# Kernel tuning notes

Measured on AMD Instinct MI355X. Metric: run time of the kernel, lower is better.

The kernel has to match this reference:

```python
import jax, jax.numpy as jnp
import numpy as np

B, T, D, H, V = 256, 32, 500, 1024, 8000
NF = 512  # conv output channels per window size


def setup_inputs() -> dict:
    key = jax.random.key(0)
    ks = jax.random.split(key, 20)
    s = 0.02
    inp = {
        "text": jax.random.normal(ks[0], (B, T, D), jnp.float32),
        "text_bow": jax.random.uniform(ks[1], (B, V), jnp.float32),
        "text_lengths": jax.random.randint(ks[2], (B,), 1, T + 1).astype(jnp.int32),
        # GRU forward direction (PyTorch layout: [3H, D], [3H, H], gates r,z,n)
        "Wih_f": jax.random.normal(ks[3], (3 * H, D), jnp.float32) * s,
        "Whh_f": jax.random.normal(ks[4], (3 * H, H), jnp.float32) * s,
        "bih_f": jax.random.normal(ks[5], (3 * H,), jnp.float32) * s,
        "bhh_f": jax.random.normal(ks[6], (3 * H,), jnp.float32) * s,
        # GRU backward direction
        "Wih_b": jax.random.normal(ks[7], (3 * H, D), jnp.float32) * s,
        "Whh_b": jax.random.normal(ks[8], (3 * H, H), jnp.float32) * s,
        "bih_b": jax.random.normal(ks[9], (3 * H,), jnp.float32) * s,
        "bhh_b": jax.random.normal(ks[10], (3 * H,), jnp.float32) * s,
        # reduce linear: 2H -> H
        "W_red": jax.random.normal(ks[11], (H, 2 * H), jnp.float32) * s,
        "b_red": jax.random.normal(ks[12], (H,), jnp.float32) * s,
        # conv kernels, reshaped from Conv2d [512,1,ws,2H] to 1D conv [512, 2H, ws]
        "conv_w2": jax.random.normal(ks[13], (NF, 2 * H, 2), jnp.float32) * s,
        "conv_b2": jax.random.normal(ks[14], (NF,), jnp.float32) * s,
        "conv_w3": jax.random.normal(ks[15], (NF, 2 * H, 3), jnp.float32) * s,
        "conv_b3": jax.random.normal(ks[16], (NF,), jnp.float32) * s,
        "conv_w4": jax.random.normal(ks[17], (NF, 2 * H, 4), jnp.float32) * s,
        "conv_b4": jax.random.normal(ks[18], (NF,), jnp.float32) * s,
    }
    return inp


def _run_gru_dir(x, lengths, Wih, Whh, bih, bhh, reverse):
    """One GRU direction over padded [B,T,D] with packed-sequence semantics:
    outputs are zero at t >= length (as pad_packed_sequence produces)."""
    b, t, _ = x.shape
    h_dim = Whh.shape[1]
    xg = jnp.einsum('btd,gd->btg', x, Wih) + bih  # [B,T,3H] input projections
    valid = jnp.arange(t)[None, :] < lengths[:, None]  # [B,T]

    def step(h, inp):
        xg_t, v = inp  # [B,3H], [B]
        hg = h @ Whh.T + bhh
        xr, xz, xn = jnp.split(xg_t, 3, axis=-1)
        hr, hz, hn = jnp.split(hg, 3, axis=-1)
        r = jax.nn.sigmoid(xr + hr)
        z = jax.nn.sigmoid(xz + hz)
        n = jnp.tanh(xn + r * hn)
        h_new = (1.0 - z) * n + z * h
        h_new = jnp.where(v[:, None], h_new, h)
        out = jnp.where(v[:, None], h_new, 0.0)
        return h_new, out

    h0 = jnp.zeros((b, h_dim), x.dtype)
    xs = (jnp.swapaxes(xg, 0, 1), valid.T)  # time-major
    _, outs = jax.lax.scan(step, h0, xs, reverse=reverse)
    return jnp.swapaxes(outs, 0, 1)  # [B,T,H]


def _conv_branch(x_c, w, b, ws):
    # x_c: [B, 2H, T]; w: [512, 2H, ws]; 'same-padding-both-sides' (ws-1) like Conv2d padding=(ws-1,0)
    y = jax.lax.conv_general_dilated(
        x_c, w, window_strides=(1,), padding=[(ws - 1, ws - 1)],
        dimension_numbers=('NCH', 'OIH', 'NCH')) + b[None, :, None]
    y = jax.nn.leaky_relu(y, 0.01)
    return jnp.max(y, axis=-1)  # global max-pool over time -> [B,512]


def reference(text, text_bow, text_lengths, Wih_f, Whh_f, bih_f, bhh_f,
              Wih_b, Whh_b, bih_b, bhh_b, W_red, b_red,
              conv_w2, conv_b2, conv_w3, conv_b3, conv_w4, conv_b4):
    out_f = _run_gru_dir(text, text_lengths, Wih_f, Whh_f, bih_f, bhh_f, reverse=False)
    out_b = _run_gru_dir(text, text_lengths, Wih_b, Whh_b, bih_b, bhh_b, reverse=True)
    gru_init_out = jnp.concatenate([out_f, out_b], axis=-1)  # [B,T,2H]

    # masked mean pooling over valid timesteps (the per-sample Python loop)
    mask = (jnp.arange(gru_init_out.shape[1])[None, :] < text_lengths[:, None]).astype(gru_init_out.dtype)
    gru_mean = jnp.sum(gru_init_out * mask[:, :, None], axis=1) / text_lengths[:, None].astype(gru_init_out.dtype)
    gru_out = gru_mean @ W_red.T + b_red  # [B,H] (dropout is identity at eval)

    x_c = jnp.swapaxes(gru_init_out, 1, 2)  # [B,2H,T]
    con_out = jnp.concatenate([
        _conv_branch(x_c, conv_w2, conv_b2, 2),
        _conv_branch(x_c, conv_w3, conv_b3, 3),
        _conv_branch(x_c, conv_w4, conv_b4, 4),
    ], axis=1)  # [B,1536]

    return jnp.concatenate([gru_out, con_out, text_bow], axis=1)  # [B, H+1536+V]
```

## Files before the change

kernel.cpp:

```cpp
#include <hip/hip_runtime.h>
#include <hip/hip_bf16.h>
#include <math.h>

#define B_ 256
#define T_ 32
#define D_ 500
#define H_ 1024
#define V_ 8000
#define NF_ 512
#define G3H (3*H_)
#define G6H (6*H_)
#define H2 (2*H_)
#define OUTC (H_ + 3*NF_ + V_)
#define KPAD 512
#define NTAP 9
#define NCAT (NTAP*NF_)
#define MS 512
#define WFRAG_G (64*32*512)
#define WHH_N (3*64*32*64)

typedef float f32x4 __attribute__((ext_vector_type(4)));
typedef short bf16x8 __attribute__((ext_vector_type(8)));

static __device__ __forceinline__ short f2b(float f) {
    unsigned u = __float_as_uint(f);
    unsigned r = (u + 0x7fffu + ((u >> 16) & 1u)) >> 16;
    return (short)r;
}
static __device__ __forceinline__ float b2f(short s) {
    return __uint_as_float(((unsigned)(unsigned short)s) << 16);
}

template<int MODE>
__global__ __launch_bounds__(256) void gemm_bt2(
    const short* __restrict__ A, int lda,
    const short* __restrict__ Bt, int ldb,
    const float* __restrict__ bias,
    void* __restrict__ Cv, int ldc, int K)
{
    __shared__ short As[3][128 * 32];
    __shared__ short Bs[3][128 * 32];
    const int tid = threadIdx.x;
    const int w = tid >> 6, lane = tid & 63;

    const int nbx = gridDim.x;
    const int nwg = nbx * gridDim.y;
    const int C = nwg >> 3;
    const int R = gridDim.y >> 3;
    const int orig = blockIdx.y * nbx + blockIdx.x;
    const int x = orig & 7;
    const int local = orig >> 3;
    const int seg = local / (R * 4);
    const int rem = local % (R * 4);
    const int mm = rem >> 2, nn = rem & 3;
    const int m0 = (x * R + mm) * 128;
    const int n0 = (seg * 4 + nn) * 128;

    const int wm = (w >> 1) * 64, wn = (w & 1) * 64;

    const int sa = lane & 1, sb = (lane >> 1) & 1, sc = (lane >> 2) & 1;
    const int sd = (lane >> 3) & 1, se = (lane >> 4) & 1, sg = (lane >> 5) & 1;
    const int srow = w * 16 + (sc ^ sg) + 2 * sd + 4 * se + 8 * sg;
    const int scol = 8 * ((sa ^ sd) + 2 * (sb ^ se));
    const long aoff0 = (long)(m0 + srow) * lda + scol;
    const long aoff1 = (long)(m0 + srow + 64) * lda + scol;
    const long boff0 = (long)(n0 + srow) * ldb + scol;
    const long boff1 = (long)(n0 + srow + 64) * ldb + scol;

#define STG(t_) do { \
    const int bu_ = (t_) % 3; \
    const long ka_ = (long)(t_) * 32; \
    __builtin_amdgcn_global_load_lds((const __attribute__((address_space(1))) void*)(A + aoff0 + ka_), \
        (__attribute__((address_space(3))) void*)(&As[bu_][w * 512]), 16, 0, 0); \
    __builtin_amdgcn_global_load_lds((const __attribute__((address_space(1))) void*)(A + aoff1 + ka_), \
        (__attribute__((address_space(3))) void*)(&As[bu_][2048 + w * 512]), 16, 0, 0); \
    __builtin_amdgcn_global_load_lds((const __attribute__((address_space(1))) void*)(Bt + boff0 + ka_), \
        (__attribute__((address_space(3))) void*)(&Bs[bu_][w * 512]), 16, 0, 0); \
    __builtin_amdgcn_global_load_lds((const __attribute__((address_space(1))) void*)(Bt + boff1 + ka_), \
        (__attribute__((address_space(3))) void*)(&Bs[bu_][2048 + w * 512]), 16, 0, 0); \
} while (0)

    f32x4 acc[4][4];
#pragma unroll
    for (int i = 0; i < 4; ++i)
#pragma unroll
        for (int j = 0; j < 4; ++j) acc[i][j] = (f32x4){0.f, 0.f, 0.f, 0.f};

    const int fr = lane & 15;
    const int fkb = (lane >> 4) * 16;
    const int fxor = ((fr >> 1) & 7) << 4;
    const int T = K >> 5;

    STG(0); STG(1);
    asm volatile("s_waitcnt vmcnt(4)" ::: "memory");
    __builtin_amdgcn_s_barrier();

    for (int t = 0; t < T; ++t) {
        const int bu = t % 3;
        const char* Ab = (const char*)&As[bu][0];
        const char* Bb = (const char*)&Bs[bu][0];

        bf16x8 af[4], bfv[4];
#pragma unroll
        for (int i = 0; i < 4; ++i)
            af[i] = *(const bf16x8*)(Ab + ((((wm + i * 16 + fr) << 6) + fkb) ^ fxor));
#pragma unroll
        for (int j = 0; j < 4; ++j)
            bfv[j] = *(const bf16x8*)(Bb + ((((wn + j * 16 + fr) << 6) + fkb) ^ fxor));

        if (t + 2 < T) STG(t + 2);

#pragma unroll
        for (int i = 0; i < 4; ++i)
#pragma unroll
            for (int j = 0; j < 4; ++j)
                acc[i][j] = __builtin_amdgcn_mfma_f32_16x16x32_bf16(af[i], bfv[j], acc[i][j], 0, 0, 0);

        if (t + 2 < T)      asm volatile("s_waitcnt vmcnt(4)" ::: "memory");
        else if (t + 1 < T) asm volatile("s_waitcnt vmcnt(0)" ::: "memory");
        __builtin_amdgcn_s_barrier();
    }
#undef STG

    const int er = (lane >> 4) * 4, ec = lane & 15;
#pragma unroll
    for (int i = 0; i < 4; ++i) {
#pragma unroll
        for (int j = 0; j < 4; ++j) {
#pragma unroll
            for (int q = 0; q < 4; ++q) {
                const int m = m0 + wm + i * 16 + er + q;
                const int n = n0 + wn + j * 16 + ec;
                const float v = acc[i][j][q];
                if (MODE == 2)
                    ((short*)Cv)[(long)m * ldc + n] = f2b(v + bias[n]);
                else
                    ((_Float16*)Cv)[(long)m * ldc + n] = (_Float16)v;
            }
        }
    }
}

__global__ __launch_bounds__(256) void gemm_bt(
    const short* __restrict__ A, int lda,
    const short* __restrict__ Bt, int ldb,
    const float* __restrict__ bias,
    void* __restrict__ Cv, int ldc,
    int K, int mode)
{
    __shared__ short As[128 * 32];
    __shared__ short Bs[128 * 32];
    const int tid  = threadIdx.x;
    const int w    = tid >> 6, lane = tid & 63;

    const int nbx = gridDim.x;
    const int nwg = nbx * gridDim.y;
    int flat = blockIdx.y * nbx + blockIdx.x;
    flat = (flat & 7) * (nwg >> 3) + (flat >> 3);
    const int m0 = (flat / nbx) * 128, n0 = (flat % nbx) * 128;

    const int wm   = (w >> 1) * 64, wn = (w & 1) * 64;

    f32x4 acc[4][4];
#pragma unroll
    for (int i = 0; i < 4; ++i)
#pragma unroll
        for (int j = 0; j < 4; ++j) acc[i][j] = (f32x4){0.f, 0.f, 0.f, 0.f};

    const int srow = w * 16 + (lane >> 2);
    const int scol = (lane & 3) * 8;
    const long aoff0 = (long)(m0 + srow) * lda + scol;
    const long aoff1 = (long)(m0 + srow + 64) * lda + scol;
    const long boff0 = (long)(n0 + srow) * ldb + scol;
    const long boff1 = (long)(n0 + srow + 64) * ldb + scol;
    short* lA0 = As + w * 512;        short* lA1 = As + 2048 + w * 512;
    short* lB0 = Bs + w * 512;        short* lB1 = Bs + 2048 + w * 512;

    const int fr = lane & 15, fk = (lane >> 4) * 8;

    for (int kt = 0; kt < K; kt += 32) {
        __builtin_amdgcn_global_load_lds((const __attribute__((address_space(1))) void*)(A + aoff0 + kt),
                                         (__attribute__((address_space(3))) void*)lA0, 16, 0, 0);
        __builtin_amdgcn_global_load_lds((const __attribute__((address_space(1))) void*)(A + aoff1 + kt),
                                         (__attribute__((address_space(3))) void*)lA1, 16, 0, 0);
        __builtin_amdgcn_global_load_lds((const __attribute__((address_space(1))) void*)(Bt + boff0 + kt),
                                         (__attribute__((address_space(3))) void*)lB0, 16, 0, 0);
        __builtin_amdgcn_global_load_lds((const __attribute__((address_space(1))) void*)(Bt + boff1 + kt),
                                         (__attribute__((address_space(3))) void*)lB1, 16, 0, 0);
        __syncthreads();
        bf16x8 af[4], bfv[4];
#pragma unroll
        for (int i = 0; i < 4; ++i) af[i]  = *(const bf16x8*)(As + (wm + i * 16 + fr) * 32 + fk);
#pragma unroll
        for (int j = 0; j < 4; ++j) bfv[j] = *(const bf16x8*)(Bs + (wn + j * 16 + fr) * 32 + fk);
#pragma unroll
        for (int i = 0; i < 4; ++i)
#pragma unroll
            for (int j = 0; j < 4; ++j)
                acc[i][j] = __builtin_amdgcn_mfma_f32_16x16x32_bf16(af[i], bfv[j], acc[i][j], 0, 0, 0);
        __syncthreads();
    }

    const int er = (lane >> 4) * 4;
    const int ec = lane & 15;
#pragma unroll
    for (int i = 0; i < 4; ++i) {
#pragma unroll
        for (int j = 0; j < 4; ++j) {
#pragma unroll
            for (int q = 0; q < 4; ++q) {
                const int m = m0 + wm + i * 16 + er + q;
                const int n = n0 + wn + j * 16 + ec;
                float v = acc[i][j][q];
                if (mode == 0) {
                    ((float*)Cv)[(long)m * ldc + n] = v + bias[n];
                } else if (mode == 2) {
                    ((short*)Cv)[(long)m * ldc + n] = f2b(v + bias[n]);
                } else {
                    ((_Float16*)Cv)[(long)m * ldc + n] = (_Float16)v;
                }
            }
        }
    }
}

__global__ void repack_whh2(const float* __restrict__ srcf,
                            const float* __restrict__ srcb,
                            short* __restrict__ dst)
{
    const int idx = blockIdx.x * 256 + threadIdx.x;
    const int h = idx >= WHH_N;
    const int local = idx - h * WHH_N;
    const float* src = h ? srcb : srcf;
    const int l = local & 63;
    const int kt = (local >> 6) & 31;
    const int j16 = (local >> 11) & 63;
    const int g = local >> 17;
    const long srow = ((long)(g << 10) + (j16 << 4) + (l & 15)) * H_ + kt * 32 + ((l >> 4) << 3);
    short o[8];
#pragma unroll
    for (int e = 0; e < 8; ++e) o[e] = f2b(src[srow + e]);
    *(bf16x8*)&dst[(long)idx * 8] = *(bf16x8*)o;
}

__global__ __launch_bounds__(512) void gru_step_frag(
    const short* __restrict__ hbf_prev, short* __restrict__ hbf_next,
    const float* __restrict__ h32_prev, float* __restrict__ h32_next,
    const short* __restrict__ wfragf, const short* __restrict__ wfragb,
    const float* __restrict__ bhhf, const float* __restrict__ bhhb,
    const short* __restrict__ xgcat,
    short* __restrict__ gout, const int* __restrict__ lengths, int s)
{
    __shared__ f32x4 lacc[4][6][64];
    const int tid = threadIdx.x;
    const int w8 = tid >> 6;
    const int w = w8 & 3;
    const int khalf = w8 >> 2;
    const int lane = tid & 63;
    const int bid = blockIdx.x;
    const int jt = bid & 31;
    const int mtd = bid >> 5;
    const int dir = mtd >> 2, mt = mtd & 3;
    const int m0 = dir * 256 + mt * 64;
    const int j0 = jt * 32;
    const int wm = (w >> 1) * 32, wj = (w & 1) * 16;
    const int tt = dir ? (T_ - 1 - s) : s;

    const short* wfrag = dir ? wfragb : wfragf;
    const float* bhh = dir ? bhhb : bhhf;

    const int fr15 = lane & 15, fk8 = (lane >> 4) * 8;
    const long arow0 = (long)(m0 + wm + fr15) * H_ + fk8 + khalf * 512;
    const long arow1 = arow0 + (long)16 * H_;
    const int j16 = (j0 + wj) >> 4;
    const short* bbase = wfrag + ((long)j16 * 32 + khalf * 16) * 512 + lane * 8;

    f32x4 acc[3][2];
#pragma unroll
    for (int g = 0; g < 3; ++g)
#pragma unroll
        for (int i = 0; i < 2; ++i) acc[g][i] = (f32x4){0.f, 0.f, 0.f, 0.f};

#pragma unroll 4
    for (int kt = 0; kt < 16; ++kt) {
        const bf16x8 af0 = *(const bf16x8*)(hbf_prev + arow0 + kt * 32);
        const bf16x8 af1 = *(const bf16x8*)(hbf_prev + arow1 + kt * 32);
        const bf16x8 b0 = *(const bf16x8*)(bbase + (long)kt * 512);
        const bf16x8 b1 = *(const bf16x8*)(bbase + (long)kt * 512 + WFRAG_G);
        const bf16x8 b2 = *(const bf16x8*)(bbase + (long)kt * 512 + 2 * WFRAG_G);
        acc[0][0] = __builtin_amdgcn_mfma_f32_16x16x32_bf16(af0, b0, acc[0][0], 0, 0, 0);
        acc[0][1] = __builtin_amdgcn_mfma_f32_16x16x32_bf16(af1, b0, acc[0][1], 0, 0, 0);
        acc[1][0] = __builtin_amdgcn_mfma_f32_16x16x32_bf16(af0, b1, acc[1][0], 0, 0, 0);
        acc[1][1] = __builtin_amdgcn_mfma_f32_16x16x32_bf16(af1, b1, acc[1][1], 0, 0, 0);
        acc[2][0] = __builtin_amdgcn_mfma_f32_16x16x32_bf16(af0, b2, acc[2][0], 0, 0, 0);
        acc[2][1] = __builtin_amdgcn_mfma_f32_16x16x32_bf16(af1, b2, acc[2][1], 0, 0, 0);
    }

    if (khalf == 1) {
#pragma unroll
        for (int g = 0; g < 3; ++g)
#pragma unroll
            for (int i = 0; i < 2; ++i)
                lacc[w][g * 2 + i][lane] = acc[g][i];
    }
    __syncthreads();
    if (khalf == 1) return;

#pragma unroll
    for (int g = 0; g < 3; ++g)
#pragma unroll
        for (int i = 0; i < 2; ++i)
            acc[g][i] += lacc[w][g * 2 + i][lane];

    const int er = (lane >> 4) * 4, ec = lane & 15;
    const int jj = j0 + wj + ec;
    const float bhr = bhh[jj], bhz = bhh[H_ + jj], bhn = bhh[2 * H_ + jj];

#pragma unroll
    for (int i = 0; i < 2; ++i) {
#pragma unroll
        for (int q = 0; q < 4; ++q) {
            const int m = m0 + wm + i * 16 + er + q;
            const int b = m & 255;
            const short* xrow = xgcat + ((long)b * T_ + tt) * G6H + (long)dir * G3H;
            const float xr = b2f(xrow[jj]);
            const float xz = b2f(xrow[H_ + jj]);
            const float xn = b2f(xrow[2 * H_ + jj]);
            const float rr = 1.f / (1.f + expf(-(xr + acc[0][i][q] + bhr)));
            const float zz = 1.f / (1.f + expf(-(xz + acc[1][i][q] + bhz)));
            const float nn = tanhf(xn + rr * (acc[2][i][q] + bhn));
            const long hidx = (long)m * H_ + jj;
            const float hp = h32_prev[hidx];
            const float hnew = (1.f - zz) * nn + zz * hp;
            const bool valid = tt < lengths[b];
            const float ho = valid ? hnew : hp;
            h32_next[hidx] = ho;
            hbf_next[hidx] = f2b(ho);
            gout[((long)b * T_ + tt) * H2 + (long)dir * H_ + jj] = valid ? f2b(hnew) : (short)0;
        }
    }
}

__global__ void f2b_pad(const float* __restrict__ src, short* __restrict__ dst,
                        int Ksrc, int Kdst)
{
    const int idx = blockIdx.x * 256 + threadIdx.x;
    const int r = idx / Kdst, c = idx % Kdst;
    dst[idx] = (c < Ksrc) ? f2b(src[(long)r * Ksrc + c]) : (short)0;
}

__global__ void wih_pad2(const float* __restrict__ a, const float* __restrict__ b,
                         short* __restrict__ dst)
{
    const int idx = blockIdx.x * 256 + threadIdx.x;
    const int h = idx >= G3H * KPAD;
    const int rem = idx - h * G3H * KPAD;
    const int r = rem / KPAD, c = rem % KPAD;
    const float* s = h ? b : a;
    dst[idx] = (c < D_) ? f2b(s[(long)r * D_ + c]) : (short)0;
}

__global__ void cat_bias(const float* __restrict__ a, const float* __restrict__ b,
                         float* __restrict__ dst)
{
    const int idx = blockIdx.x * 256 + threadIdx.x;
    dst[idx] = (idx < G3H) ? a[idx] : b[idx - G3H];
}

__global__ void repack_tap_all(const float* __restrict__ cw2,
                               const float* __restrict__ cw3,
                               const float* __restrict__ cw4,
                               short* __restrict__ dst)
{
    const int idx = blockIdx.x * 256 + threadIdx.x;
    const int tap = idx / (NF_ * H2);
    const int rem = idx % (NF_ * H2);
    const int f = rem >> 11, c = rem & 2047;
    const float* src; int ws, k;
    if (tap < 2)      { src = cw2; ws = 2; k = tap; }
    else if (tap < 5) { src = cw3; ws = 3; k = tap - 2; }
    else              { src = cw4; ws = 4; k = tap - 5; }
    dst[idx] = f2b(src[((long)(f << 11) + c) * ws + k]);
}

__global__ void mean_pool2(const short* __restrict__ gin,
                           const int* __restrict__ lengths,
                           short* __restrict__ mean_bf)
{
    const int idx = blockIdx.x * 256 + threadIdx.x;
    const int b = idx >> 11, c = idx & 2047;
    float s = 0.f;
#pragma unroll
    for (int t = 0; t < T_; ++t) s += b2f(gin[((long)(b * T_ + t)) * H2 + c]);
    mean_bf[idx] = f2b(s / (float)lengths[b]);
}

__global__ void conv_max(const _Float16* __restrict__ P,
                         const float* __restrict__ cb2, const float* __restrict__ cb3,
                         const float* __restrict__ cb4, float* __restrict__ out)
{
    const int idx = blockIdx.x * 256 + threadIdx.x;
    const int b = idx / 1536, u0 = idx % 1536;
    int Tout, ws, base, f; float bias;
    if (u0 < 512)       { ws = 2; Tout = 33; base = 0;    f = u0;        bias = cb2[f]; }
    else if (u0 < 1024) { ws = 3; Tout = 34; base = 1024; f = u0 - 512;  bias = cb3[f]; }
    else                { ws = 4; Tout = 35; base = 2560; f = u0 - 1024; bias = cb4[f]; }
    const _Float16* Pb = P + (long)b * T_ * NCAT + base + f;
    float m = -INFINITY;
    for (int u = 0; u < Tout; ++u) {
        float s = bias;
        for (int k = 0; k < ws; ++k) {
            const int t = u - (ws - 1) + k;
            if (t >= 0 && t < T_) s += (float)Pb[(long)t * NCAT + k * NF_];
        }
        s = s > 0.f ? s : 0.01f * s;
        m = fmaxf(m, s);
    }
    out[(long)b * OUTC + H_ + u0] = m;
}

__global__ void bow_copy(const float* __restrict__ bow, float* __restrict__ out)
{
    const int idx = blockIdx.x * 256 + threadIdx.x;
    const int b = idx / 2000, q = idx % 2000;
    const float4* src = (const float4*)(bow + (long)b * V_);
    float4* dst = (float4*)(out + (long)b * OUTC + H_ + 3 * NF_);
    dst[q] = src[q];
}

extern "C" void kernel_launch(void* const* d_in, const int* in_sizes, int n_in,
                              void* d_out, int out_size, void* d_ws, size_t ws_size,
                              hipStream_t stream)
{
    const float* text    = (const float*)d_in[0];
    const float* bow     = (const float*)d_in[1];
    const int*   lengths = (const int*)  d_in[2];
    const float* Wih_f   = (const float*)d_in[3];
    const float* Whh_f   = (const float*)d_in[4];
    const float* bih_f   = (const float*)d_in[5];
    const float* bhh_f   = (const float*)d_in[6];
    const float* Wih_b   = (const float*)d_in[7];
    const float* Whh_b   = (const float*)d_in[8];
    const float* bih_b   = (const float*)d_in[9];
    const float* bhh_b   = (const float*)d_in[10];
    const float* W_red   = (const float*)d_in[11];
    const float* b_red   = (const float*)d_in[12];
    const float* cw2     = (const float*)d_in[13];
    const float* cb2     = (const float*)d_in[14];
    const float* cw3     = (const float*)d_in[15];
    const float* cb3     = (const float*)d_in[16];
    const float* cw4     = (const float*)d_in[17];
    const float* cb4     = (const float*)d_in[18];
    float* out = (float*)d_out;

    char* ws = (char*)d_ws;
    size_t off = 0;
    short* xgcat = (short*)(ws + off); off += (size_t)B_ * T_ * G6H * 2;
    _Float16* P    = (_Float16*)(char*)xgcat;
    short* wtap_bf = (short*)((char*)xgcat + (size_t)B_ * T_ * NCAT * 2);
    short* gin_bf = (short*)(ws + off); off += (size_t)B_ * T_ * H2 * 2;
    short* text_bf = gin_bf;
    short* wih_bf  = (short*)((char*)gin_bf + (size_t)B_ * T_ * KPAD * 2);
    short* wfrag   = (short*)(ws + off); off += (size_t)2 * 3 * WFRAG_G * 2;
    short* wfragf  = wfrag;
    short* wfragb  = wfrag + (size_t)3 * WFRAG_G;
    short* wred_bf = (short*)(ws + off); off += (size_t)H_ * H2 * 2;
    float* h32     = (float*)(ws + off); off += (size_t)2 * MS * H_ * 4;
    short* h_bf    = (short*)(ws + off); off += (size_t)2 * MS * H_ * 2;
    short* gmean_bf= (short*)(ws + off); off += (size_t)B_ * H2 * 2;
    float* bih_cat = (float*)(ws + off); off += (size_t)G6H * 4;

    const dim3 blk(256);

    f2b_pad<<<dim3((B_ * T_ * KPAD) / 256), blk, 0, stream>>>(text, text_bf, D_, KPAD);
    wih_pad2<<<dim3((2 * G3H * KPAD) / 256), blk, 0, stream>>>(Wih_f, Wih_b, wih_bf);
    f2b_pad<<<dim3((H_ * H2) / 256), blk, 0, stream>>>(W_red, wred_bf, H2, H2);
    cat_bias<<<dim3(G6H / 256), blk, 0, stream>>>(bih_f, bih_b, bih_cat);
    repack_whh2<<<dim3((2 * WHH_N) / 256), blk, 0, stream>>>(Whh_f, Whh_b, wfrag);

    gemm_bt2<2><<<dim3(G6H / 128, (B_ * T_) / 128), blk, 0, stream>>>(
        text_bf, KPAD, wih_bf, KPAD, bih_cat, xgcat, G6H, KPAD);

    hipMemsetAsync(h32, 0, (size_t)MS * H_ * 4, stream);
    hipMemsetAsync(h_bf, 0, (size_t)MS * H_ * 2, stream);
    for (int s = 0; s < T_; ++s) {
        const int cur = s & 1, nxt = (s + 1) & 1;
        gru_step_frag<<<dim3(256), dim3(512), 0, stream>>>(
            h_bf + (size_t)cur * MS * H_, h_bf + (size_t)nxt * MS * H_,
            h32 + (size_t)cur * MS * H_, h32 + (size_t)nxt * MS * H_,
            wfragf, wfragb, bhh_f, bhh_b, xgcat,
            gin_bf, lengths, s);
    }

    mean_pool2<<<dim3((B_ * H2) / 256), blk, 0, stream>>>(gin_bf, lengths, gmean_bf);
    gemm_bt<<<dim3(H_ / 128, B_ / 128), blk, 0, stream>>>(
        gmean_bf, H2, wred_bf, H2, b_red, out, OUTC, H2, 0);

    repack_tap_all<<<dim3((NTAP * NF_ * H2) / 256), blk, 0, stream>>>(cw2, cw3, cw4, wtap_bf);
    gemm_bt2<3><<<dim3(NCAT / 128, (B_ * T_) / 128), blk, 0, stream>>>(
        gin_bf, H2, wtap_bf, H2, nullptr, P, NCAT, H2);

    conv_max<<<dim3((B_ * 1536) / 256), blk, 0, stream>>>(P, cb2, cb3, cb4, out);
    bow_copy<<<dim3((B_ * 2000) / 256), blk, 0, stream>>>(bow, out);
}
```

Baseline: 951.0 us.

## Enlarge bf16 MFMA GEMM tiles to 256x256 with 512-thread blocks

Replaces the 128x128, 256-thread triple-buffered GEMM with a 256x256, 512-thread version. Each of the 8 waves now computes a 128x64 sub-tile (8x4 MFMA fragments), and the block-swizzle mapping is changed to groups of 3 N-tiles. Both the input projection GEMM and the conv tap GEMM use the new kernel. The aim is more data reuse per LDS load and fewer global loads. In exchange it needs more registers and 96KB of LDS, and the grid has fewer blocks (e.g. 24x32 and 18x32), which may hurt occupancy or tail balance.

```diff
diff --git a/kernel.cpp b/kernel.cpp
--- a/kernel.cpp
+++ b/kernel.cpp
@@ -32,57 +32,56 @@
 }
 
 template<int MODE>
-__global__ __launch_bounds__(256) void gemm_bt2(
+__global__ __launch_bounds__(512) void gemm256r(
     const short* __restrict__ A, int lda,
     const short* __restrict__ Bt, int ldb,
     const float* __restrict__ bias,
     void* __restrict__ Cv, int ldc, int K)
 {
-    __shared__ short As[3][128 * 32];
-    __shared__ short Bs[3][128 * 32];
+    __shared__ short As[3][256 * 32];
+    __shared__ short Bs[3][256 * 32];
     const int tid = threadIdx.x;
     const int w = tid >> 6, lane = tid & 63;
 
     const int nbx = gridDim.x;
-    const int nwg = nbx * gridDim.y;
-    const int C = nwg >> 3;
     const int R = gridDim.y >> 3;
     const int orig = blockIdx.y * nbx + blockIdx.x;
     const int x = orig & 7;
     const int local = orig >> 3;
-    const int seg = local / (R * 4);
-    const int rem = local % (R * 4);
-    const int mm = rem >> 2, nn = rem & 3;
-    const int m0 = (x * R + mm) * 128;
-    const int n0 = (seg * 4 + nn) * 128;
-
-    const int wm = (w >> 1) * 64, wn = (w & 1) * 64;
+    const int seg = local / (R * 3);
+    const int rem = local % (R * 3);
+    const int mm = rem / 3, nn = rem % 3;
+    const int m0 = (x * R + mm) * 256;
+    const int n0 = (seg * 3 + nn) * 256;
+
+    const int wm = (w >> 2) * 128;
+    const int wn = (w & 3) * 64;
 
     const int sa = lane & 1, sb = (lane >> 1) & 1, sc = (lane >> 2) & 1;
     const int sd = (lane >> 3) & 1, se = (lane >> 4) & 1, sg = (lane >> 5) & 1;
-    const int srow = w * 16 + (sc ^ sg) + 2 * sd + 4 * se + 8 * sg;
+    const int srow16 = (sc ^ sg) + 2 * sd + 4 * se + 8 * sg;
     const int scol = 8 * ((sa ^ sd) + 2 * (sb ^ se));
-    const long aoff0 = (long)(m0 + srow) * lda + scol;
-    const long aoff1 = (long)(m0 + srow + 64) * lda + scol;
-    const long boff0 = (long)(n0 + srow) * ldb + scol;
-    const long boff1 = (long)(n0 + srow + 64) * ldb + scol;
+    const long aoff0 = (long)(m0 + w * 32 + srow16) * lda + scol;
+    const long aoff1 = (long)(m0 + w * 32 + 16 + srow16) * lda + scol;
+    const long boff0 = (long)(n0 + w * 32 + srow16) * ldb + scol;
+    const long boff1 = (long)(n0 + w * 32 + 16 + srow16) * ldb + scol;
 
 #define STG(t_) do { \
     const int bu_ = (t_) % 3; \
     const long ka_ = (long)(t_) * 32; \
     __builtin_amdgcn_global_load_lds((const __attribute__((address_space(1))) void*)(A + aoff0 + ka_), \
-        (__attribute__((address_space(3))) void*)(&As[bu_][w * 512]), 16, 0, 0); \
+        (__attribute__((address_space(3))) void*)(&As[bu_][(w * 32) * 32]), 16, 0, 0); \
     __builtin_amdgcn_global_load_lds((const __attribute__((address_space(1))) void*)(A + aoff1 + ka_), \
-        (__attribute__((address_space(3))) void*)(&As[bu_][2048 + w * 512]), 16, 0, 0); \
+        (__attribute__((address_space(3))) void*)(&As[bu_][(w * 32 + 16) * 32]), 16, 0, 0); \
     __builtin_amdgcn_global_load_lds((const __attribute__((address_space(1))) void*)(Bt + boff0 + ka_), \
-        (__attribute__((address_space(3))) void*)(&Bs[bu_][w * 512]), 16, 0, 0); \
+        (__attribute__((address_space(3))) void*)(&Bs[bu_][(w * 32) * 32]), 16, 0, 0); \
     __builtin_amdgcn_global_load_lds((const __attribute__((address_space(1))) void*)(Bt + boff1 + ka_), \
-        (__attribute__((address_space(3))) void*)(&Bs[bu_][2048 + w * 512]), 16, 0, 0); \
+        (__attribute__((address_space(3))) void*)(&Bs[bu_][(w * 32 + 16) * 32]), 16, 0, 0); \
 } while (0)
 
-    f32x4 acc[4][4];
-#pragma unroll
-    for (int i = 0; i < 4; ++i)
+    f32x4 acc[8][4];
+#pragma unroll
+    for (int i = 0; i < 8; ++i)
 #pragma unroll
         for (int j = 0; j < 4; ++j) acc[i][j] = (f32x4){0.f, 0.f, 0.f, 0.f};
 
@@ -100,9 +99,9 @@
         const char* Ab = (const char*)&As[bu][0];
         const char* Bb = (const char*)&Bs[bu][0];
 
-        bf16x8 af[4], bfv[4];
-#pragma unroll
-        for (int i = 0; i < 4; ++i)
+        bf16x8 af[8], bfv[4];
+#pragma unroll
+        for (int i = 0; i < 8; ++i)
             af[i] = *(const bf16x8*)(Ab + ((((wm + i * 16 + fr) << 6) + fkb) ^ fxor));
 #pragma unroll
         for (int j = 0; j < 4; ++j)
@@ -111,7 +110,7 @@
         if (t + 2 < T) STG(t + 2);
 
 #pragma unroll
-        for (int i = 0; i < 4; ++i)
+        for (int i = 0; i < 8; ++i)
 #pragma unroll
             for (int j = 0; j < 4; ++j)
                 acc[i][j] = __builtin_amdgcn_mfma_f32_16x16x32_bf16(af[i], bfv[j], acc[i][j], 0, 0, 0);
@@ -124,7 +123,7 @@
 
     const int er = (lane >> 4) * 4, ec = lane & 15;
 #pragma unroll
-    for (int i = 0; i < 4; ++i) {
+    for (int i = 0; i < 8; ++i) {
 #pragma unroll
         for (int j = 0; j < 4; ++j) {
 #pragma unroll
@@ -478,7 +477,7 @@
     cat_bias<<<dim3(G6H / 256), blk, 0, stream>>>(bih_f, bih_b, bih_cat);
     repack_whh2<<<dim3((2 * WHH_N) / 256), blk, 0, stream>>>(Whh_f, Whh_b, wfrag);
 
-    gemm_bt2<2><<<dim3(G6H / 128, (B_ * T_) / 128), blk, 0, stream>>>(
+    gemm256r<2><<<dim3(G6H / 256, (B_ * T_) / 256), dim3(512), 0, stream>>>(
         text_bf, KPAD, wih_bf, KPAD, bih_cat, xgcat, G6H, KPAD);
 
     hipMemsetAsync(h32, 0, (size_t)MS * H_ * 4, stream);
@@ -497,7 +496,7 @@
         gmean_bf, H2, wred_bf, H2, b_red, out, OUTC, H2, 0);
 
     repack_tap_all<<<dim3((NTAP * NF_ * H2) / 256), blk, 0, stream>>>(cw2, cw3, cw4, wtap_bf);
-    gemm_bt2<3><<<dim3(NCAT / 128, (B_ * T_) / 128), blk, 0, stream>>>(
+    gemm256r<3><<<dim3(NCAT / 256, (B_ * T_) / 256), dim3(512), 0, stream>>>(
         gin_bf, H2, wtap_bf, H2, nullptr, P, NCAT, H2);
 
     conv_max<<<dim3((B_ * 1536) / 256), blk, 0, stream>>>(P, cb2, cb3, cb4, out);
```

New measurement: 944.0 us. About the same (-0.7%).
